# Optimization experiments

Measured on AMD Instinct MI355X. Metric: run time of the kernel, lower is better.

The kernel has to match this reference:

```python
import jax, jax.numpy as jnp
import numpy as np

BETA = 0.25  # commitment weight from config['beta']


def _mlp(h, ws, bs):
    # MLPLayers: Linear + ReLU between hidden layers, no activation after last.
    n = len(ws)
    for i in range(n):
        h = h @ ws[i] + bs[i]
        if i < n - 1:
            h = jax.nn.relu(h)
    return h


def setup_inputs() -> dict:
    key = jax.random.key(0)
    ks = jax.random.split(key, 16)
    B, IN = 65536, 768
    dims = [768, 512, 256, 128]  # [in_dim] + layers + [e_dim]
    d = {"x": jax.random.normal(ks[0], (B, IN), dtype=jnp.float32)}
    # encoder weights
    for i in range(3):
        fan_in = dims[i]
        d[f"enc_w{i}"] = jax.random.normal(ks[1 + i], (dims[i], dims[i + 1]), dtype=jnp.float32) / np.sqrt(fan_in)
        d[f"enc_b{i}"] = jnp.zeros((dims[i + 1],), dtype=jnp.float32)
    rdims = dims[::-1]
    for i in range(3):
        d[f"dec_w{i}"] = jax.random.normal(ks[4 + i], (rdims[i], rdims[i + 1]), dtype=jnp.float32) / np.sqrt(rdims[i])
        d[f"dec_b{i}"] = jnp.zeros((rdims[i + 1],), dtype=jnp.float32)
    # 4 residual levels, 256 codes each, e_dim=128
    d["codebooks"] = jax.random.normal(ks[7], (4, 256, 128), dtype=jnp.float32)
    return d


def reference(x, enc_w0, enc_b0, enc_w1, enc_b1, enc_w2, enc_b2,
              dec_w0, dec_b0, dec_w1, dec_b1, dec_w2, dec_b2, codebooks):
    sg = jax.lax.stop_gradient
    z = _mlp(x, [enc_w0, enc_w1, enc_w2], [enc_b0, enc_b1, enc_b2])  # (B, e_dim)

    residual = z
    x_q = jnp.zeros_like(z)
    losses = []
    n_levels = codebooks.shape[0]
    for l in range(n_levels):
        C = codebooks[l]  # (K, e_dim)
        # squared L2 distances (B, K) via expansion, avoids materializing diffs
        dist = (jnp.sum(residual * residual, axis=1, keepdims=True)
                - 2.0 * residual @ C.T
                + jnp.sum(C * C, axis=1))
        idx = jnp.argmin(dist, axis=1)  # (B,)
        q = C[idx]                      # (B, e_dim) gather
        # codebook loss + beta * commitment loss
        losses.append(jnp.mean((sg(q) - residual) ** 2)
                      + BETA * jnp.mean((q - sg(residual)) ** 2))
        x_q = x_q + q
        residual = residual - sg(q)
    rq_loss = jnp.mean(jnp.stack(losses))

    # straight-through estimator
    y_q = z + sg(x_q - z)
    y = _mlp(y_q, [dec_w0, dec_w1, dec_w2], [dec_b0, dec_b1, dec_b2])  # (B, in_dim)
    return y, rq_loss
```

## Files before the change

### kernel.cpp

```cpp
#include <hip/hip_runtime.h>
#include <cstdint>
#include <cstddef>


typedef _Float16 F16;
typedef F16   v8h  __attribute__((ext_vector_type(8)));
typedef F16   v2h  __attribute__((ext_vector_type(2)));
typedef F16   v4h  __attribute__((ext_vector_type(4)));
typedef float v4f  __attribute__((ext_vector_type(4)));

__device__ __forceinline__ void gload_lds16(const void* g, void* l) {
    __builtin_amdgcn_global_load_lds(
        (const __attribute__((address_space(1))) void*)g,
        (__attribute__((address_space(3))) void*)l, 16, 0, 0);
}

__device__ __forceinline__ void split2(float v, F16& h, F16& l) {
    h = (F16)v;
    l = (F16)((v - (float)h) * 2048.0f);
}

template<bool RELU, bool HASBIAS, bool WF32, bool WSPLIT>
__global__ __launch_bounds__(256, 2)
void f16gemm2(const F16* __restrict__ Ah, const F16* __restrict__ Al,
              const F16* __restrict__ Bh, const F16* __restrict__ Bl,
              const float* __restrict__ bias,
              float* __restrict__ C, F16* __restrict__ Ch, F16* __restrict__ Cl,
              int N, int K, int nbn)
{
    __shared__ v8h As[2048];
    __shared__ v8h Bs[2048];

    const int tid  = threadIdx.x;
    const int lane = tid & 63;
    const int wid  = tid >> 6;

    const int nb  = gridDim.x;
    const int cpx = nb >> 3;
    const int sw  = (blockIdx.x & 7) * cpx + (blockIdx.x >> 3);
    const int mt  = sw / nbn;
    const int nt_ = sw - mt * nbn;
    const long bm = (long)mt * 128;
    const long bn = (long)nt_ * 128;

    const int rr = lane >> 3;
    const int c  = (lane & 7) ^ rr;
    const F16* aS[4]; const F16* bS[4];
    int dOf[4];
    #pragma unroll
    for (int jj = 0; jj < 4; jj++) {
        int rloc = wid * 32 + jj * 8;
        long ag = bm + rloc + rr, bg = bn + rloc + rr;
        aS[jj] = (c < 4) ? (Ah + ag * (long)K + c * 8) : (Al + ag * (long)K + (c - 4) * 8);
        bS[jj] = (c < 4) ? (Bh + bg * (long)K + c * 8) : (Bl + bg * (long)K + (c - 4) * 8);
        dOf[jj] = rloc * 8;
    }

    const int cq = lane >> 4;
    const int wr = wid >> 1, wc = wid & 1;
    int aOff[4], bOff[4];
    #pragma unroll
    for (int i = 0; i < 4; i++) {
        int am  = wr * 64 + i * 16 + (lane & 15);
        aOff[i] = am * 8 + (cq ^ (am & 7));
        int bn2 = wc * 64 + i * 16 + (lane & 15);
        bOff[i] = bn2 * 8 + (cq ^ (bn2 & 7));
    }

    v4f acc[4][4]  = {};
    v4f accx[4][4] = {};

    auto stage = [&](int buf, int k0) {
        v8h* Ab = As + buf * 1024;
        v8h* Bb = Bs + buf * 1024;
        #pragma unroll
        for (int jj = 0; jj < 4; jj++) gload_lds16(aS[jj] + k0, Ab + dOf[jj]);
        #pragma unroll
        for (int jj = 0; jj < 4; jj++) gload_lds16(bS[jj] + k0, Bb + dOf[jj]);
    };

    const int nsteps = K >> 5;
    stage(0, 0);
    __syncthreads();

    for (int t = 0; t < nsteps; ++t) {
        const int cur = t & 1;
        if (t + 1 < nsteps) stage(cur ^ 1, (t + 1) * 32);

        const v8h* Ab = As + cur * 1024;
        const v8h* Bb = Bs + cur * 1024;
        v8h ah[4], al[4], bh[4], bl[4];
        #pragma unroll
        for (int i = 0; i < 4; i++) {
            ah[i] = Ab[aOff[i]]; al[i] = Ab[aOff[i] ^ 4];
            bh[i] = Bb[bOff[i]]; bl[i] = Bb[bOff[i] ^ 4];
        }
        #pragma unroll
        for (int mi = 0; mi < 4; mi++)
            #pragma unroll
            for (int ni = 0; ni < 4; ni++) {
                acc[mi][ni]  = __builtin_amdgcn_mfma_f32_16x16x32_f16(ah[mi], bh[ni], acc[mi][ni],  0, 0, 0);
                accx[mi][ni] = __builtin_amdgcn_mfma_f32_16x16x32_f16(ah[mi], bl[ni], accx[mi][ni], 0, 0, 0);
                accx[mi][ni] = __builtin_amdgcn_mfma_f32_16x16x32_f16(al[mi], bh[ni], accx[mi][ni], 0, 0, 0);
            }
        __syncthreads();
    }

    const int rbase = (lane >> 4) * 4;
    const int cl    = lane & 15;
    #pragma unroll
    for (int ni = 0; ni < 4; ni++) {
        long col = bn + wc * 64 + ni * 16 + cl;
        float bv = 0.0f;
        if constexpr (HASBIAS) bv = bias[col];
        #pragma unroll
        for (int mi = 0; mi < 4; mi++) {
            #pragma unroll
            for (int r = 0; r < 4; r++) {
                long row = bm + wr * 64 + mi * 16 + rbase + r;
                float v = acc[mi][ni][r] + accx[mi][ni][r] * (1.0f / 2048.0f) + bv;
                if constexpr (RELU) v = fmaxf(v, 0.0f);
                if constexpr (WF32) C[row * (long)N + col] = v;
                if constexpr (WSPLIT) {
                    F16 h, l; split2(v, h, l);
                    Ch[row * (long)N + col] = h;
                    Cl[row * (long)N + col] = l;
                }
            }
        }
    }
}

__global__ void wprep_kernel(const float* __restrict__ W, F16* __restrict__ H,
                             F16* __restrict__ L, int K, int N)
{
    int i = blockIdx.x * 256 + threadIdx.x;
    if (i >= K * N) return;
    int k = i / N, n = i % N;
    float v = W[i];
    F16 h, l; split2(v, h, l);
    H[(long)n * K + k] = h;
    L[(long)n * K + k] = l;
}

__global__ void cbprep_kernel(const float* __restrict__ Cb, F16* __restrict__ H,
                              F16* __restrict__ L)
{
    int i = blockIdx.x * 256 + threadIdx.x;
    float v = Cb[i];
    F16 h, l; split2(v, h, l);
    H[i] = h; L[i] = l;
}

__global__ void xsplit_kernel(const float* __restrict__ X, F16* __restrict__ H,
                              F16* __restrict__ L, long n4)
{
    long stride = (long)gridDim.x * 256;
    for (long i = blockIdx.x * 256 + threadIdx.x; i < n4; i += stride) {
        float4 v = reinterpret_cast<const float4*>(X)[i];
        v4h h, l; F16 hh, ll;
        split2(v.x, hh, ll); h[0] = hh; l[0] = ll;
        split2(v.y, hh, ll); h[1] = hh; l[1] = ll;
        split2(v.z, hh, ll); h[2] = hh; l[2] = ll;
        split2(v.w, hh, ll); h[3] = hh; l[3] = ll;
        reinterpret_cast<v4h*>(H)[i] = h;
        reinterpret_cast<v4h*>(L)[i] = l;
    }
}

__global__ __launch_bounds__(256)
void rq_update_kernel(const float* __restrict__ scores,
                      const float* __restrict__ cb,
                      const float* __restrict__ src,
                      float* __restrict__ resid,
                      F16* __restrict__ residh, F16* __restrict__ residl,
                      float* __restrict__ xq,
                      F16* __restrict__ xqh, F16* __restrict__ xql,
                      float* __restrict__ lossF,
                      int M, int first, int last)
{
    __shared__ float c2s[256];
    __shared__ float lsum[4];
    const int tid  = threadIdx.x;
    const int lane = tid & 63;
    const int wave = tid >> 6;

    {   float s = 0.f;
        #pragma unroll
        for (int d = 0; d < 128; d += 4) {
            float4 v = *reinterpret_cast<const float4*>(cb + (long)tid * 128 + d);
            s += v.x * v.x + v.y * v.y + v.z * v.z + v.w * v.w;
        }
        c2s[tid] = s;
    }
    __syncthreads();

    float myloss = 0.f;
    const int stride = gridDim.x * 4;
    for (int row = blockIdx.x * 4 + wave; row < M; row += stride) {
        const float* srow = scores + (long)row * 256;
        float best = 3.4e38f; int bidx = 0;
        #pragma unroll
        for (int j = 0; j < 4; j++) {
            int code = lane + j * 64;
            float d = fmaf(-2.f, srow[code], c2s[code]);
            if (d < best) { best = d; bidx = code; }
        }
        #pragma unroll
        for (int off = 32; off > 0; off >>= 1) {
            float ob = __shfl_down(best, off);
            int   oi = __shfl_down(bidx, off);
            if (ob < best || (ob == best && oi < bidx)) { best = ob; bidx = oi; }
        }
        bidx = __shfl(bidx, 0);

        long base = (long)row * 128 + lane * 2;
        float2 r = *reinterpret_cast<const float2*>(src + base);
        float2 q = *reinterpret_cast<const float2*>(cb + (long)bidx * 128 + lane * 2);
        float dx = r.x - q.x, dy = r.y - q.y;
        myloss += dx * dx + dy * dy;

        if (!last) {
            float2 nr; nr.x = dx; nr.y = dy;
            *reinterpret_cast<float2*>(resid + base) = nr;
            v2h nh, nl; F16 h, l;
            split2(dx, h, l); nh[0] = h; nl[0] = l;
            split2(dy, h, l); nh[1] = h; nl[1] = l;
            *reinterpret_cast<v2h*>(residh + base) = nh;
            *reinterpret_cast<v2h*>(residl + base) = nl;
        }
        float2 xv;
        if (first) { xv.x = q.x; xv.y = q.y; }
        else {
            xv = *reinterpret_cast<float2*>(xq + base);
            xv.x += q.x; xv.y += q.y;
        }
        if (!last) {
            *reinterpret_cast<float2*>(xq + base) = xv;
        } else {
            v2h nh, nl; F16 h, l;
            split2(xv.x, h, l); nh[0] = h; nl[0] = l;
            split2(xv.y, h, l); nh[1] = h; nl[1] = l;
            *reinterpret_cast<v2h*>(xqh + base) = nh;
            *reinterpret_cast<v2h*>(xql + base) = nl;
        }
    }

    #pragma unroll
    for (int off = 32; off > 0; off >>= 1) myloss += __shfl_down(myloss, off);
    if (lane == 0) lsum[wave] = myloss;
    __syncthreads();
    if (tid == 0) atomicAdd(lossF, (lsum[0] + lsum[1]) + (lsum[2] + lsum[3]));
}

__global__ void zero4_kernel(float* __restrict__ F)
{
    if (threadIdx.x < 4) F[threadIdx.x] = 0.f;
}

__global__ void finalize_loss_kernel(const float* __restrict__ F, float* __restrict__ out)
{
    if (threadIdx.x == 0) {
        float s = (F[0] + F[1]) + (F[2] + F[3]);
        out[0] = s * (1.25f / (4.f * 65536.f * 128.f));
    }
}

extern "C" void kernel_launch(void* const* d_in, const int* in_sizes, int n_in,
                              void* d_out, int out_size, void* d_ws, size_t ws_size,
                              hipStream_t stream)
{
    const float* x      = (const float*)d_in[0];
    const float* enc_w0 = (const float*)d_in[1];
    const float* enc_b0 = (const float*)d_in[2];
    const float* enc_w1 = (const float*)d_in[3];
    const float* enc_b1 = (const float*)d_in[4];
    const float* enc_w2 = (const float*)d_in[5];
    const float* enc_b2 = (const float*)d_in[6];
    const float* dec_w0 = (const float*)d_in[7];
    const float* dec_b0 = (const float*)d_in[8];
    const float* dec_w1 = (const float*)d_in[9];
    const float* dec_b1 = (const float*)d_in[10];
    const float* dec_w2 = (const float*)d_in[11];
    const float* dec_b2 = (const float*)d_in[12];
    const float* codebooks = (const float*)d_in[13];

    const int M = 65536;

    F16*   wsF = (F16*)d_ws;
    float* wsf = (float*)d_ws;
    F16*   Xh  = wsF;
    F16*   Xl  = wsF + 50331648;
    float* z   = wsf;
    F16*   zh  = wsF + 16777216;
    F16*   zl  = wsF + 25165824;
    F16*   g2l = wsF;
    F16*   g2h = wsF + 33554432;
    F16*   h2h = wsF + 67108864;
    F16*   h2l = wsF + 83886080;
    float* scores = wsf + 33554432;
    F16*   g1h = wsF + 67108864;
    F16*   g1l = wsF + 83886080;
    F16*   d2h = wsF + 67108864;
    F16*   d2l = d2h + 393216;

    F16*   doF = (F16*)d_out;
    float* y   = (float*)d_out;
    F16*   h1h = doF;
    F16*   h1l = doF + 33554432;
    float* xq  = (float*)d_out;
    F16*   xqh = doF + 16777216;
    F16*   xql = doF + 25165824;
    F16*   w_  = doF + 67108864;
    F16* e0h = w_;              F16* e0l = e0h + 393216;
    F16* e1h = e0l + 393216;    F16* e1l = e1h + 131072;
    F16* e2h = e1l + 131072;    F16* e2l = e2h + 32768;
    F16* d0h = e2l + 32768;     F16* d0l = d0h + 32768;
    F16* d1h = d0l + 32768;     F16* d1l = d1h + 131072;
    F16* cbh = d1l + 131072;    F16* cbl = cbh + 131072;
    float* F = (float*)d_out + 35000000;

    dim3 blk(256);

    wprep_kernel<<<dim3(1536), blk, 0, stream>>>(enc_w0, e0h, e0l, 768, 512);
    wprep_kernel<<<dim3(512),  blk, 0, stream>>>(enc_w1, e1h, e1l, 512, 256);
    wprep_kernel<<<dim3(128),  blk, 0, stream>>>(enc_w2, e2h, e2l, 256, 128);
    wprep_kernel<<<dim3(128),  blk, 0, stream>>>(dec_w0, d0h, d0l, 128, 256);
    wprep_kernel<<<dim3(512),  blk, 0, stream>>>(dec_w1, d1h, d1l, 256, 512);
    cbprep_kernel<<<dim3(512), blk, 0, stream>>>(codebooks, cbh, cbl);
    xsplit_kernel<<<dim3(4096), blk, 0, stream>>>(x, Xh, Xl, 12582912);
    zero4_kernel<<<dim3(1), dim3(64), 0, stream>>>(F);

    f16gemm2<true,  true, false, true ><<<dim3(2048), blk, 0, stream>>>(Xh, Xl, e0h, e0l, enc_b0, nullptr, h1h, h1l, 512, 768, 4);
    f16gemm2<true,  true, false, true ><<<dim3(1024), blk, 0, stream>>>(h1h, h1l, e1h, e1l, enc_b1, nullptr, h2h, h2l, 256, 512, 2);
    f16gemm2<false, true, true,  true ><<<dim3(512),  blk, 0, stream>>>(h2h, h2l, e2h, e2l, enc_b2, z, zh, zl, 128, 256, 1);

    for (int l = 0; l < 4; l++) {
        const float* cb = codebooks + (long)l * 32768;
        const float* src = (l == 0) ? z : z;
        f16gemm2<false, false, true, false><<<dim3(1024), blk, 0, stream>>>(zh, zl, cbh + l * 32768, cbl + l * 32768,
                                                                            nullptr, scores, nullptr, nullptr, 256, 128, 2);
        rq_update_kernel<<<dim3(1024), blk, 0, stream>>>(scores, cb, src, z, zh, zl, xq, xqh, xql,
                                                         F + l, M, (l == 0) ? 1 : 0, (l == 3) ? 1 : 0);
    }
    finalize_loss_kernel<<<dim3(1), dim3(64), 0, stream>>>(F, y + 50331648);

    f16gemm2<true,  true, false, true ><<<dim3(1024), blk, 0, stream>>>(xqh, xql, d0h, d0l, dec_b0, nullptr, g1h, g1l, 256, 128, 2);
    f16gemm2<true,  true, false, true ><<<dim3(2048), blk, 0, stream>>>(g1h, g1l, d1h, d1l, dec_b1, nullptr, g2h, g2l, 512, 256, 4);
    wprep_kernel<<<dim3(1536), blk, 0, stream>>>(dec_w2, d2h, d2l, 512, 768);
    f16gemm2<false, true, true,  false><<<dim3(3072), blk, 0, stream>>>(g2h, g2l, d2h, d2l, dec_b2, y, nullptr, nullptr, 768, 512, 6);
}
```

Measured before the change: 1.311 ms.

## Fuse argmin into codebook GEMM, stage epilogue through LDS, merge prep kernels

The codebook-distance GEMM now computes distances and a per-row argmin over each 128-code tile in its epilogue. It writes only two candidates per row instead of the full 65536x256 score matrix, and the update kernel picks between them. Other GEMM epilogues go through LDS and emit vectorized float4/half4 stores, and the K loop uses explicit vmcnt waits, raw barriers and setprio around the MFMAs. All the weight, codebook, x-split, codebook-norm and zeroing prep kernels are merged into one launch. The cost is a larger LDS allocation per block, which may limit occupancy, plus more complex synchronization.

```diff
diff --git a/kernel.cpp b/kernel.cpp
--- a/kernel.cpp
+++ b/kernel.cpp
@@ -20,23 +20,24 @@
     l = (F16)((v - (float)h) * 2048.0f);
 }
 
-template<bool RELU, bool HASBIAS, bool WF32, bool WSPLIT>
+template<int OUT, bool RELU, bool HASBIAS>
 __global__ __launch_bounds__(256, 2)
-void f16gemm2(const F16* __restrict__ Ah, const F16* __restrict__ Al,
+void f16gemm3(const F16* __restrict__ Ah, const F16* __restrict__ Al,
               const F16* __restrict__ Bh, const F16* __restrict__ Bl,
               const float* __restrict__ bias,
               float* __restrict__ C, F16* __restrict__ Ch, F16* __restrict__ Cl,
+              const float* __restrict__ c2, float2* __restrict__ cand,
               int N, int K, int nbn)
 {
-    __shared__ v8h As[2048];
-    __shared__ v8h Bs[2048];
+    __shared__ __attribute__((aligned(16))) char smem[67584];
+    v8h* As = (v8h*)smem;
+    v8h* Bs = (v8h*)(smem + 32768);
 
     const int tid  = threadIdx.x;
     const int lane = tid & 63;
     const int wid  = tid >> 6;
 
-    const int nb  = gridDim.x;
-    const int cpx = nb >> 3;
+    const int cpx = gridDim.x >> 3;
     const int sw  = (blockIdx.x & 7) * cpx + (blockIdx.x >> 3);
     const int mt  = sw / nbn;
     const int nt_ = sw - mt * nbn;
@@ -81,11 +82,18 @@
 
     const int nsteps = K >> 5;
     stage(0, 0);
-    __syncthreads();
 
     for (int t = 0; t < nsteps; ++t) {
         const int cur = t & 1;
-        if (t + 1 < nsteps) stage(cur ^ 1, (t + 1) * 32);
+        if (t + 1 < nsteps) {
+            stage(cur ^ 1, (t + 1) * 32);
+            asm volatile("s_waitcnt vmcnt(8)" ::: "memory");
+        } else {
+            asm volatile("s_waitcnt vmcnt(0)" ::: "memory");
+        }
+        __builtin_amdgcn_sched_barrier(0);
+        __builtin_amdgcn_s_barrier();
+        __builtin_amdgcn_sched_barrier(0);
 
         const v8h* Ab = As + cur * 1024;
         const v8h* Bb = Bs + cur * 1024;
@@ -95,6 +103,7 @@
             ah[i] = Ab[aOff[i]]; al[i] = Ab[aOff[i] ^ 4];
             bh[i] = Bb[bOff[i]]; bl[i] = Bb[bOff[i] ^ 4];
         }
+        __builtin_amdgcn_s_setprio(1);
         #pragma unroll
         for (int mi = 0; mi < 4; mi++)
             #pragma unroll
@@ -103,31 +112,166 @@
                 accx[mi][ni] = __builtin_amdgcn_mfma_f32_16x16x32_f16(ah[mi], bl[ni], accx[mi][ni], 0, 0, 0);
                 accx[mi][ni] = __builtin_amdgcn_mfma_f32_16x16x32_f16(al[mi], bh[ni], accx[mi][ni], 0, 0, 0);
             }
-        __syncthreads();
-    }
-
-    const int rbase = (lane >> 4) * 4;
-    const int cl    = lane & 15;
-    #pragma unroll
-    for (int ni = 0; ni < 4; ni++) {
-        long col = bn + wc * 64 + ni * 16 + cl;
-        float bv = 0.0f;
-        if constexpr (HASBIAS) bv = bias[col];
-        #pragma unroll
-        for (int mi = 0; mi < 4; mi++) {
+        __builtin_amdgcn_s_setprio(0);
+        __builtin_amdgcn_sched_barrier(0);
+        __builtin_amdgcn_s_barrier();
+        __builtin_amdgcn_sched_barrier(0);
+    }
+
+    const int cl = lane & 15;
+    const int rb = (lane >> 4) * 4;
+
+    if constexpr (OUT == 3) {
+        float* cD = (float*)smem;
+        int*   cI = (int*)(smem + 1024);
+        float bd[4][4]; int bi[4][4];
+        #pragma unroll
+        for (int mi = 0; mi < 4; mi++)
             #pragma unroll
             for (int r = 0; r < 4; r++) {
-                long row = bm + wr * 64 + mi * 16 + rbase + r;
-                float v = acc[mi][ni][r] + accx[mi][ni][r] * (1.0f / 2048.0f) + bv;
-                if constexpr (RELU) v = fmaxf(v, 0.0f);
-                if constexpr (WF32) C[row * (long)N + col] = v;
-                if constexpr (WSPLIT) {
-                    F16 h, l; split2(v, h, l);
-                    Ch[row * (long)N + col] = h;
-                    Cl[row * (long)N + col] = l;
+                float bb = 3.4e38f; int ii = 0;
+                #pragma unroll
+                for (int ni = 0; ni < 4; ni++) {
+                    int code = (int)bn + wc * 64 + ni * 16 + cl;
+                    float s  = acc[mi][ni][r] + accx[mi][ni][r] * (1.0f / 2048.0f);
+                    float d  = fmaf(-2.0f, s, c2[code]);
+                    if (d < bb || (d == bb && code < ii)) { bb = d; ii = code; }
                 }
+                bd[mi][r] = bb; bi[mi][r] = ii;
             }
-        }
+        #pragma unroll
+        for (int off = 1; off < 16; off <<= 1)
+            #pragma unroll
+            for (int mi = 0; mi < 4; mi++)
+                #pragma unroll
+                for (int r = 0; r < 4; r++) {
+                    float od = __shfl_xor(bd[mi][r], off);
+                    int   oi = __shfl_xor(bi[mi][r], off);
+                    if (od < bd[mi][r] || (od == bd[mi][r] && oi < bi[mi][r])) {
+                        bd[mi][r] = od; bi[mi][r] = oi;
+                    }
+                }
+        if (cl == 0)
+            #pragma unroll
+            for (int mi = 0; mi < 4; mi++)
+                #pragma unroll
+                for (int r = 0; r < 4; r++) {
+                    int rl = wr * 64 + mi * 16 + rb + r;
+                    cD[rl * 2 + wc] = bd[mi][r];
+                    cI[rl * 2 + wc] = bi[mi][r];
+                }
+        __syncthreads();
+        if (tid < 128) {
+            float d0 = cD[tid * 2], d1 = cD[tid * 2 + 1];
+            int   i0 = cI[tid * 2], i1 = cI[tid * 2 + 1];
+            float pd; int pk;
+            if (d1 < d0 || (d1 == d0 && i1 < i0)) { pd = d1; pk = i1; }
+            else                                  { pd = d0; pk = i0; }
+            float2 out; out.x = pd; out.y = __int_as_float(pk);
+            cand[(bm + tid) * 2 + (bn >> 7)] = out;
+        }
+    } else {
+        float* sC = (float*)smem;
+        #pragma unroll
+        for (int mi = 0; mi < 4; mi++)
+            #pragma unroll
+            for (int ni = 0; ni < 4; ni++)
+                #pragma unroll
+                for (int r = 0; r < 4; r++)
+                    sC[(wr * 64 + mi * 16 + rb + r) * 132 + wc * 64 + ni * 16 + cl] =
+                        acc[mi][ni][r] + accx[mi][ni][r] * (1.0f / 2048.0f);
+        __syncthreads();
+        const int trow = tid >> 5;
+        const int tcol = (tid & 31) << 2;
+        float4 bv = {0.f, 0.f, 0.f, 0.f};
+        if constexpr (HASBIAS) bv = *reinterpret_cast<const float4*>(bias + bn + tcol);
+        #pragma unroll
+        for (int it = 0; it < 16; ++it) {
+            int row = trow + it * 8;
+            float4 v = *reinterpret_cast<const float4*>(&sC[row * 132 + tcol]);
+            v.x += bv.x; v.y += bv.y; v.z += bv.z; v.w += bv.w;
+            if constexpr (RELU) {
+                v.x = fmaxf(v.x, 0.f); v.y = fmaxf(v.y, 0.f);
+                v.z = fmaxf(v.z, 0.f); v.w = fmaxf(v.w, 0.f);
+            }
+            long gr = (bm + row) * (long)N + bn + tcol;
+            if constexpr (OUT == 0 || OUT == 2)
+                *reinterpret_cast<float4*>(C + gr) = v;
+            if constexpr (OUT == 1 || OUT == 2) {
+                v4h h4, l4; F16 h, l;
+                split2(v.x, h, l); h4[0] = h; l4[0] = l;
+                split2(v.y, h, l); h4[1] = h; l4[1] = l;
+                split2(v.z, h, l); h4[2] = h; l4[2] = l;
+                split2(v.w, h, l); h4[3] = h; l4[3] = l;
+                *reinterpret_cast<v4h*>(Ch + gr) = h4;
+                *reinterpret_cast<v4h*>(Cl + gr) = l4;
+            }
+        }
+    }
+}
+
+__device__ __forceinline__ void wprep_task(const float* __restrict__ W,
+                                           F16* __restrict__ H, F16* __restrict__ L,
+                                           int K, int N, int idx, int stride, int total)
+{
+    for (int i = idx; i < total; i += stride) {
+        int k = i / N, n = i - k * N;
+        float v = W[i];
+        F16 h, l; split2(v, h, l);
+        H[(long)n * K + k] = h;
+        L[(long)n * K + k] = l;
+    }
+}
+
+__global__ __launch_bounds__(256)
+void prep_all(const float* __restrict__ x,
+              const float* __restrict__ ew0, const float* __restrict__ ew1,
+              const float* __restrict__ ew2, const float* __restrict__ dw0,
+              const float* __restrict__ dw1, const float* __restrict__ cball,
+              F16* __restrict__ Xh, F16* __restrict__ Xl,
+              F16* __restrict__ e0h, F16* __restrict__ e0l,
+              F16* __restrict__ e1h, F16* __restrict__ e1l,
+              F16* __restrict__ e2h, F16* __restrict__ e2l,
+              F16* __restrict__ d0h, F16* __restrict__ d0l,
+              F16* __restrict__ d1h, F16* __restrict__ d1l,
+              F16* __restrict__ cbh, F16* __restrict__ cbl,
+              float* __restrict__ c2all, float* __restrict__ F)
+{
+    const int b = blockIdx.x, t = threadIdx.x;
+    if (b < 3072) {
+        for (long i = (long)b * 256 + t; i < 12582912; i += 786432) {
+            float4 v = reinterpret_cast<const float4*>(x)[i];
+            v4h h4, l4; F16 h, l;
+            split2(v.x, h, l); h4[0] = h; l4[0] = l;
+            split2(v.y, h, l); h4[1] = h; l4[1] = l;
+            split2(v.z, h, l); h4[2] = h; l4[2] = l;
+            split2(v.w, h, l); h4[3] = h; l4[3] = l;
+            reinterpret_cast<v4h*>(Xh)[i] = h4;
+            reinterpret_cast<v4h*>(Xl)[i] = l4;
+        }
+    } else if (b < 3584) wprep_task(ew0, e0h, e0l, 768, 512, (b - 3072) * 256 + t, 131072, 393216);
+    else if (b < 3712)   wprep_task(ew1, e1h, e1l, 512, 256, (b - 3584) * 256 + t, 32768, 131072);
+    else if (b < 3744)   wprep_task(ew2, e2h, e2l, 256, 128, (b - 3712) * 256 + t, 8192, 32768);
+    else if (b < 3776)   wprep_task(dw0, d0h, d0l, 128, 256, (b - 3744) * 256 + t, 8192, 32768);
+    else if (b < 3904)   wprep_task(dw1, d1h, d1l, 256, 512, (b - 3776) * 256 + t, 32768, 131072);
+    else if (b < 4032) {
+        for (int i = (b - 3904) * 256 + t; i < 131072; i += 32768) {
+            float v = cball[i];
+            F16 h, l; split2(v, h, l);
+            cbh[i] = h; cbl[i] = l;
+        }
+    } else if (b < 4036) {
+        int i = (b - 4032) * 256 + t;
+        const float* row = cball + (long)i * 128;
+        float s = 0.f;
+        #pragma unroll
+        for (int d = 0; d < 128; d += 4) {
+            float4 v = *reinterpret_cast<const float4*>(row + d);
+            s += v.x * v.x + v.y * v.y + v.z * v.z + v.w * v.w;
+        }
+        c2all[i] = s;
+    } else {
+        if (t < 4) F[t] = 0.f;
     }
 }
 
@@ -136,83 +280,32 @@
 {
     int i = blockIdx.x * 256 + threadIdx.x;
     if (i >= K * N) return;
-    int k = i / N, n = i % N;
-    float v = W[i];
-    F16 h, l; split2(v, h, l);
-    H[(long)n * K + k] = h;
-    L[(long)n * K + k] = l;
-}
-
-__global__ void cbprep_kernel(const float* __restrict__ Cb, F16* __restrict__ H,
-                              F16* __restrict__ L)
-{
-    int i = blockIdx.x * 256 + threadIdx.x;
-    float v = Cb[i];
-    F16 h, l; split2(v, h, l);
-    H[i] = h; L[i] = l;
-}
-
-__global__ void xsplit_kernel(const float* __restrict__ X, F16* __restrict__ H,
-                              F16* __restrict__ L, long n4)
-{
-    long stride = (long)gridDim.x * 256;
-    for (long i = blockIdx.x * 256 + threadIdx.x; i < n4; i += stride) {
-        float4 v = reinterpret_cast<const float4*>(X)[i];
-        v4h h, l; F16 hh, ll;
-        split2(v.x, hh, ll); h[0] = hh; l[0] = ll;
-        split2(v.y, hh, ll); h[1] = hh; l[1] = ll;
-        split2(v.z, hh, ll); h[2] = hh; l[2] = ll;
-        split2(v.w, hh, ll); h[3] = hh; l[3] = ll;
-        reinterpret_cast<v4h*>(H)[i] = h;
-        reinterpret_cast<v4h*>(L)[i] = l;
-    }
+    wprep_task(W, H, L, K, N, i, K * N, i + 1);
 }
 
 __global__ __launch_bounds__(256)
-void rq_update_kernel(const float* __restrict__ scores,
-                      const float* __restrict__ cb,
-                      const float* __restrict__ src,
-                      float* __restrict__ resid,
-                      F16* __restrict__ residh, F16* __restrict__ residl,
-                      float* __restrict__ xq,
-                      F16* __restrict__ xqh, F16* __restrict__ xql,
-                      float* __restrict__ lossF,
-                      int M, int first, int last)
-{
-    __shared__ float c2s[256];
+void rq_update2(const float2* __restrict__ cand,
+                const float* __restrict__ cb,
+                const float* __restrict__ src,
+                float* __restrict__ resid,
+                F16* __restrict__ residh, F16* __restrict__ residl,
+                float* __restrict__ xq,
+                F16* __restrict__ xqh, F16* __restrict__ xql,
+                float* __restrict__ lossF,
+                int M, int first, int last)
+{
     __shared__ float lsum[4];
     const int tid  = threadIdx.x;
     const int lane = tid & 63;
     const int wave = tid >> 6;
 
-    {   float s = 0.f;
-        #pragma unroll
-        for (int d = 0; d < 128; d += 4) {
-            float4 v = *reinterpret_cast<const float4*>(cb + (long)tid * 128 + d);
-            s += v.x * v.x + v.y * v.y + v.z * v.z + v.w * v.w;
-        }
-        c2s[tid] = s;
-    }
-    __syncthreads();
-
     float myloss = 0.f;
     const int stride = gridDim.x * 4;
     for (int row = blockIdx.x * 4 + wave; row < M; row += stride) {
-        const float* srow = scores + (long)row * 256;
-        float best = 3.4e38f; int bidx = 0;
-        #pragma unroll
-        for (int j = 0; j < 4; j++) {
-            int code = lane + j * 64;
-            float d = fmaf(-2.f, srow[code], c2s[code]);
-            if (d < best) { best = d; bidx = code; }
-        }
-        #pragma unroll
-        for (int off = 32; off > 0; off >>= 1) {
-            float ob = __shfl_down(best, off);
-            int   oi = __shfl_down(bidx, off);
-            if (ob < best || (ob == best && oi < bidx)) { best = ob; bidx = oi; }
-        }
-        bidx = __shfl(bidx, 0);
+        float2 c0 = cand[(long)row * 2];
+        float2 c1 = cand[(long)row * 2 + 1];
+        int i0 = __float_as_int(c0.y), i1 = __float_as_int(c1.y);
+        int bidx = (c1.x < c0.x || (c1.x == c0.x && i1 < i0)) ? i1 : i0;
 
         long base = (long)row * 128 + lane * 2;
         float2 r = *reinterpret_cast<const float2*>(src + base);
@@ -251,11 +344,6 @@
     if (lane == 0) lsum[wave] = myloss;
     __syncthreads();
     if (tid == 0) atomicAdd(lossF, (lsum[0] + lsum[1]) + (lsum[2] + lsum[3]));
-}
-
-__global__ void zero4_kernel(float* __restrict__ F)
-{
-    if (threadIdx.x < 4) F[threadIdx.x] = 0.f;
 }
 
 __global__ void finalize_loss_kernel(const float* __restrict__ F, float* __restrict__ out)
@@ -298,7 +386,6 @@
     F16*   g2h = wsF + 33554432;
     F16*   h2h = wsF + 67108864;
     F16*   h2l = wsF + 83886080;
-    float* scores = wsf + 33554432;
     F16*   g1h = wsF + 67108864;
     F16*   g1l = wsF + 83886080;
     F16*   d2h = wsF + 67108864;
@@ -311,42 +398,39 @@
     float* xq  = (float*)d_out;
     F16*   xqh = doF + 16777216;
     F16*   xql = doF + 25165824;
-    F16*   w_  = doF + 67108864;
-    F16* e0h = w_;              F16* e0l = e0h + 393216;
+    F16* e0h = doF + 67108864;  F16* e0l = e0h + 393216;
     F16* e1h = e0l + 393216;    F16* e1l = e1h + 131072;
     F16* e2h = e1l + 131072;    F16* e2l = e2h + 32768;
     F16* d0h = e2l + 32768;     F16* d0l = d0h + 32768;
     F16* d1h = d0l + 32768;     F16* d1l = d1h + 131072;
     F16* cbh = d1l + 131072;    F16* cbl = cbh + 131072;
-    float* F = (float*)d_out + 35000000;
+    float2* cand  = (float2*)(doF + 68812800);
+    float*  c2all = (float*)(doF + 69337088);
+    float*  F     = c2all + 1024;
 
     dim3 blk(256);
 
-    wprep_kernel<<<dim3(1536), blk, 0, stream>>>(enc_w0, e0h, e0l, 768, 512);
-    wprep_kernel<<<dim3(512),  blk, 0, stream>>>(enc_w1, e1h, e1l, 512, 256);
-    wprep_kernel<<<dim3(128),  blk, 0, stream>>>(enc_w2, e2h, e2l, 256, 128);
-    wprep_kernel<<<dim3(128),  blk, 0, stream>>>(dec_w0, d0h, d0l, 128, 256);
-    wprep_kernel<<<dim3(512),  blk, 0, stream>>>(dec_w1, d1h, d1l, 256, 512);
-    cbprep_kernel<<<dim3(512), blk, 0, stream>>>(codebooks, cbh, cbl);
-    xsplit_kernel<<<dim3(4096), blk, 0, stream>>>(x, Xh, Xl, 12582912);
-    zero4_kernel<<<dim3(1), dim3(64), 0, stream>>>(F);
-
-    f16gemm2<true,  true, false, true ><<<dim3(2048), blk, 0, stream>>>(Xh, Xl, e0h, e0l, enc_b0, nullptr, h1h, h1l, 512, 768, 4);
-    f16gemm2<true,  true, false, true ><<<dim3(1024), blk, 0, stream>>>(h1h, h1l, e1h, e1l, enc_b1, nullptr, h2h, h2l, 256, 512, 2);
-    f16gemm2<false, true, true,  true ><<<dim3(512),  blk, 0, stream>>>(h2h, h2l, e2h, e2l, enc_b2, z, zh, zl, 128, 256, 1);
+    prep_all<<<dim3(4037), blk, 0, stream>>>(x, enc_w0, enc_w1, enc_w2, dec_w0, dec_w1,
+                                             codebooks, Xh, Xl, e0h, e0l, e1h, e1l,
+                                             e2h, e2l, d0h, d0l, d1h, d1l, cbh, cbl,
+                                             c2all, F);
+
+    f16gemm3<1, true,  true><<<dim3(2048), blk, 0, stream>>>(Xh, Xl, e0h, e0l, enc_b0, nullptr, h1h, h1l, nullptr, nullptr, 512, 768, 4);
+    f16gemm3<1, true,  true><<<dim3(1024), blk, 0, stream>>>(h1h, h1l, e1h, e1l, enc_b1, nullptr, h2h, h2l, nullptr, nullptr, 256, 512, 2);
+    f16gemm3<2, false, true><<<dim3(512),  blk, 0, stream>>>(h2h, h2l, e2h, e2l, enc_b2, z, zh, zl, nullptr, nullptr, 128, 256, 1);
 
     for (int l = 0; l < 4; l++) {
         const float* cb = codebooks + (long)l * 32768;
-        const float* src = (l == 0) ? z : z;
-        f16gemm2<false, false, true, false><<<dim3(1024), blk, 0, stream>>>(zh, zl, cbh + l * 32768, cbl + l * 32768,
-                                                                            nullptr, scores, nullptr, nullptr, 256, 128, 2);
-        rq_update_kernel<<<dim3(1024), blk, 0, stream>>>(scores, cb, src, z, zh, zl, xq, xqh, xql,
-                                                         F + l, M, (l == 0) ? 1 : 0, (l == 3) ? 1 : 0);
+        f16gemm3<3, false, false><<<dim3(1024), blk, 0, stream>>>(zh, zl, cbh + l * 32768, cbl + l * 32768,
+                                                                  nullptr, nullptr, nullptr, nullptr,
+                                                                  c2all + l * 256, cand, 256, 128, 2);
+        rq_update2<<<dim3(1024), blk, 0, stream>>>(cand, cb, z, z, zh, zl, xq, xqh, xql,
+                                                   F + l, M, (l == 0) ? 1 : 0, (l == 3) ? 1 : 0);
     }
     finalize_loss_kernel<<<dim3(1), dim3(64), 0, stream>>>(F, y + 50331648);
 
-    f16gemm2<true,  true, false, true ><<<dim3(1024), blk, 0, stream>>>(xqh, xql, d0h, d0l, dec_b0, nullptr, g1h, g1l, 256, 128, 2);
-    f16gemm2<true,  true, false, true ><<<dim3(2048), blk, 0, stream>>>(g1h, g1l, d1h, d1l, dec_b1, nullptr, g2h, g2l, 512, 256, 4);
+    f16gemm3<1, true,  true><<<dim3(1024), blk, 0, stream>>>(xqh, xql, d0h, d0l, dec_b0, nullptr, g1h, g1l, nullptr, nullptr, 256, 128, 2);
+    f16gemm3<1, true,  true><<<dim3(2048), blk, 0, stream>>>(g1h, g1l, d1h, d1l, dec_b1, nullptr, g2h, g2l, nullptr, nullptr, 512, 256, 4);
     wprep_kernel<<<dim3(1536), blk, 0, stream>>>(dec_w2, d2h, d2l, 512, 768);
-    f16gemm2<false, true, true,  false><<<dim3(3072), blk, 0, stream>>>(g2h, g2l, d2h, d2l, dec_b2, y, nullptr, nullptr, 768, 512, 6);
-}
+    f16gemm3<0, false, true><<<dim3(3072), blk, 0, stream>>>(g2h, g2l, d2h, d2l, dec_b2, y, nullptr, nullptr, nullptr, nullptr, 768, 512, 6);
+}
```

Result: faster. 1.147 ms (-12.5%).
